# Kernel tuning notes

Measured on AMD Instinct MI355X. Metric: run time of the kernel, lower is better.

## Reference

```python
import jax, jax.numpy as jnp
import numpy as np
from jax import lax

B, T, EPROJS, DUNITS, ATT_DIM = 32, 2048, 1024, 1024, 512
ACONV_CHANS, ACONV_FILTS = 10, 100
KSIZE = 2 * ACONV_FILTS + 1  # 201
SCALING = 2.0


def setup_inputs() -> dict:
    key = jax.random.key(0)
    ks = jax.random.split(key, 16)
    lengths = jax.random.randint(ks[1], (B,), T // 2, T + 1, dtype=jnp.int32)
    # normalized uniform initial attention over valid frames (as in module's init branch)
    mask = jnp.arange(T)[None, :] < lengths[:, None]
    att_prev = mask.astype(jnp.float32) / lengths[:, None].astype(jnp.float32)
    s_e = 1.0 / np.sqrt(EPROJS)
    s_d = 1.0 / np.sqrt(DUNITS)
    s_a = 1.0 / np.sqrt(ATT_DIM)
    s_c = 1.0 / np.sqrt(ACONV_CHANS)
    return {
        "enc_hs_pad": jax.random.normal(ks[0], (B, T, EPROJS), jnp.float32),
        "enc_hs_len": lengths,
        "dec_z": jax.random.normal(ks[2], (B, DUNITS), jnp.float32),
        "att_prev": att_prev,
        "att_h": jax.random.normal(ks[3], (B, ATT_DIM), jnp.float32) * 0.1,
        "att_c": jax.random.normal(ks[4], (B, ATT_DIM), jnp.float32) * 0.1,
        "W_enc": jax.random.uniform(ks[5], (EPROJS, ATT_DIM), jnp.float32, -s_e, s_e),
        "b_enc": jax.random.uniform(ks[6], (ATT_DIM,), jnp.float32, -s_e, s_e),
        "W_dec": jax.random.uniform(ks[7], (DUNITS, ATT_DIM), jnp.float32, -s_d, s_d),
        "W_conv": jax.random.uniform(ks[8], (ACONV_CHANS, 1, KSIZE), jnp.float32, -0.1, 0.1),
        "W_ih": jax.random.uniform(ks[9], (4 * ATT_DIM, ACONV_CHANS), jnp.float32, -s_a, s_a),
        "W_hh": jax.random.uniform(ks[10], (4 * ATT_DIM, ATT_DIM), jnp.float32, -s_a, s_a),
        "W_g": jax.random.uniform(ks[11], (ATT_DIM, 1), jnp.float32, -s_a, s_a),
        "b_g": jax.random.uniform(ks[12], (1,), jnp.float32, -s_a, s_a),
    }


def reference(enc_hs_pad, enc_hs_len, dec_z, att_prev, att_h, att_c,
              W_enc, b_enc, W_dec, W_conv, W_ih, W_hh, W_g, b_g):
    # pre_compute_enc_h = mlp_enc(enc_h): (B, T, A)
    pre_enc = jnp.einsum("bte,ea->bta", enc_hs_pad, W_enc) + b_enc

    # location conv over previous attention: (B,1,T) -> (B,C,T)
    conv = lax.conv_general_dilated(
        att_prev[:, None, :], W_conv,
        window_strides=(1,), padding=[(ACONV_FILTS, ACONV_FILTS)],
        dimension_numbers=("NCH", "OIH", "NCH"))
    # relu + global max-pool over T -> (B, C)
    conv_feat = jnp.max(jax.nn.relu(conv), axis=2)

    # LSTMCell (no bias), PyTorch gate order i, f, g, o
    gates = conv_feat @ W_ih.T + att_h @ W_hh.T  # (B, 4A)
    i, f, g, o = jnp.split(gates, 4, axis=1)
    c_new = jax.nn.sigmoid(f) * att_c + jax.nn.sigmoid(i) * jnp.tanh(g)
    h_new = jax.nn.sigmoid(o) * jnp.tanh(c_new)

    dec_t = dec_z @ W_dec  # (B, A)
    # scoring: gvec(tanh(att_h + pre_enc + dec)) -> (B, T)
    e = (jnp.tanh(h_new[:, None, :] + pre_enc + dec_t[:, None, :]) @ W_g)[..., 0] + b_g[0]

    pad_mask = jnp.arange(e.shape[1])[None, :] >= enc_hs_len[:, None]
    e = jnp.where(pad_mask, -jnp.inf, e)
    w = jax.nn.softmax(SCALING * e, axis=1)  # (B, T)

    c = jnp.einsum("bt,bte->be", w, enc_hs_pad)  # (B, EPROJS)
    return c, w, h_new, c_new
```

## Files before the change

### kernel.cpp

```cpp
#include <hip/hip_runtime.h>
#include <hip/hip_bf16.h>
#include <cstddef>

#define BB      32
#define TT_ALL  2048
#define EPROJS  1024
#define DUNITS  1024
#define ATT     512
#define CH      10
#define KS      201
#define FILT    100

#define OFF_C   0
#define OFF_W   (BB*EPROJS)
#define OFF_H   (OFF_W + BB*TT_ALL)
#define OFF_CN  (OFF_H + BB*ATT)

#define WS_CF    0
#define WS_V     512
#define WS_E     16896
#define WS_WF    82432
#define WS_WT    147968
#define WS_PART  410112
#define WS_GP    672256
#define WS_DP    803328

typedef __attribute__((ext_vector_type(8))) short short8;
typedef __attribute__((ext_vector_type(4))) float f32x4;

__device__ __forceinline__ float sigm(float x) { return 1.f / (1.f + expf(-x)); }
__device__ __forceinline__ unsigned short f2bf(float f) {
  unsigned u = __float_as_uint(f);
  return (unsigned short)((u + 0x7FFFu + ((u >> 16) & 1u)) >> 16);
}
__device__ __forceinline__ ushort2 f2bf2(float a, float b) {
  __hip_bfloat162 h = __float22bfloat162_rn(float2{a, b});
  return *reinterpret_cast<ushort2*>(&h);
}

__global__ __launch_bounds__(64) void k_wprepF(const float* __restrict__ W,
                                               unsigned short* __restrict__ WTF) {
  const int r16 = blockIdx.x >> 5, ks = blockIdx.x & 31;
  const int l = threadIdx.x;
  const int a = r16 * 16 + (l & 15);
  const int e0 = ks * 32 + (l >> 4) * 8;
  union { short8 s; unsigned short h[8]; } r;
#pragma unroll
  for (int j = 0; j < 8; ++j) r.h[j] = f2bf(W[(size_t)(e0 + j) * ATT + a]);
  *reinterpret_cast<short8*>(&WTF[((size_t)(r16 * 32 + ks) * 64 + l) * 8]) = r.s;
}

__global__ __launch_bounds__(256) void k_conv(const float* __restrict__ att_prev,
                                              const float* __restrict__ W_conv,
                                              float* __restrict__ conv_feat) {
  const int b  = blockIdx.x / CH;
  const int ch = blockIdx.x % CH;
  __shared__ float sprev[TT_ALL + 2 * FILT];
  __shared__ float sw[KS];
  __shared__ float red[4];
  const int tid = threadIdx.x;
  for (int i = tid; i < TT_ALL + 2 * FILT; i += 256) {
    int t = i - FILT;
    sprev[i] = (t >= 0 && t < TT_ALL) ? att_prev[b * TT_ALL + t] : 0.f;
  }
  for (int i = tid; i < KS; i += 256) sw[i] = W_conv[ch * KS + i];
  __syncthreads();
  float m = 0.f;
  for (int t = tid; t < TT_ALL; t += 256) {
    float s = 0.f;
    for (int k = 0; k < KS; ++k) s = fmaf(sprev[t + k], sw[k], s);
    m = fmaxf(m, s);
  }
  for (int off = 32; off; off >>= 1) m = fmaxf(m, __shfl_xor(m, off, 64));
  if ((tid & 63) == 0) red[tid >> 6] = m;
  __syncthreads();
  if (tid == 0)
    conv_feat[b * CH + ch] = fmaxf(fmaxf(red[0], red[1]), fmaxf(red[2], red[3]));
}

__global__ __launch_bounds__(256) void k_gates(const float* __restrict__ att_h,
                                               const float* __restrict__ W_hh,
                                               float* __restrict__ gp) {
  const int jt = blockIdx.x >> 1;
  const int sp = blockIdx.x & 1;
  const int j0 = jt * 64;
  const int k0 = sp * 256;
  const int tid = threadIdx.x;
  const int al = tid & 63, bg = tid >> 6;
  __shared__ float sW[64][65];
  __shared__ float sH[32][64];
  float acc[8];
#pragma unroll
  for (int i = 0; i < 8; ++i) acc[i] = 0.f;
  for (int kc = 0; kc < 256; kc += 64) {
    __syncthreads();
#pragma unroll
    for (int i = 0; i < 4; ++i) {
      const int f = tid + i * 256;
      const int r = f >> 4, q = f & 15;
      const float4 w4 = *reinterpret_cast<const float4*>(
          &W_hh[(size_t)(j0 + r) * ATT + k0 + kc + q * 4]);
      sW[r][q * 4 + 0] = w4.x; sW[r][q * 4 + 1] = w4.y;
      sW[r][q * 4 + 2] = w4.z; sW[r][q * 4 + 3] = w4.w;
    }
#pragma unroll
    for (int i = 0; i < 2; ++i) {
      const int g = tid + i * 256;
      const int r = g >> 4, q = g & 15;
      *reinterpret_cast<float4*>(&sH[r][q * 4]) = *reinterpret_cast<const float4*>(
          &att_h[(size_t)r * ATT + k0 + kc + q * 4]);
    }
    __syncthreads();
#pragma unroll 16
    for (int k = 0; k < 64; ++k) {
      const float w = sW[al][k];
#pragma unroll
      for (int bb = 0; bb < 8; ++bb)
        acc[bb] = fmaf(w, sH[bg * 8 + bb][k], acc[bb]);
    }
  }
#pragma unroll
  for (int bb = 0; bb < 8; ++bb)
    gp[((size_t)(sp * 32 + bg * 8 + bb)) * (4 * ATT) + j0 + al] = acc[bb];
}

__global__ __launch_bounds__(256) void k_dec(const float* __restrict__ dec_z,
                                             const float* __restrict__ W_dec,
                                             float* __restrict__ dp) {
  const int at = blockIdx.x >> 1;
  const int sp = blockIdx.x & 1;
  const int a0 = at * 64;
  const int d0 = sp * 512;
  const int tid = threadIdx.x;
  const int al = tid & 63, bg = tid >> 6;
  __shared__ float sW[64][64];
  __shared__ float sZ[32][64];
  float acc[8];
#pragma unroll
  for (int i = 0; i < 8; ++i) acc[i] = 0.f;
  for (int dc = 0; dc < 512; dc += 64) {
    __syncthreads();
#pragma unroll
    for (int i = 0; i < 4; ++i) {
      const int f = tid + i * 256;
      const int r = f >> 4, q = f & 15;
      *reinterpret_cast<float4*>(&sW[r][q * 4]) = *reinterpret_cast<const float4*>(
          &W_dec[(size_t)(d0 + dc + r) * ATT + a0 + q * 4]);
    }
#pragma unroll
    for (int i = 0; i < 2; ++i) {
      const int g = tid + i * 256;
      const int r = g >> 4, q = g & 15;
      *reinterpret_cast<float4*>(&sZ[r][q * 4]) = *reinterpret_cast<const float4*>(
          &dec_z[(size_t)r * DUNITS + d0 + dc + q * 4]);
    }
    __syncthreads();
#pragma unroll 16
    for (int d = 0; d < 64; ++d) {
      const float w = sW[d][al];
#pragma unroll
      for (int bb = 0; bb < 8; ++bb)
        acc[bb] = fmaf(sZ[bg * 8 + bb][d], w, acc[bb]);
    }
  }
#pragma unroll
  for (int bb = 0; bb < 8; ++bb)
    dp[((size_t)(sp * 32 + bg * 8 + bb)) * ATT + a0 + al] = acc[bb];
}

__global__ __launch_bounds__(256) void k_lstm_v(const float* __restrict__ gp,
                                                const float* __restrict__ dp,
                                                const float* __restrict__ conv_feat,
                                                const float* __restrict__ W_ih,
                                                const float* __restrict__ att_c,
                                                float* __restrict__ v,
                                                float* __restrict__ out) {
  const int b = blockIdx.x, tid = threadIdx.x;
  __shared__ float scf[CH];
  if (tid < CH) scf[tid] = conv_feat[b * CH + tid];
  __syncthreads();
  for (int a = tid; a < ATT; a += 256) {
    float g4[4];
#pragma unroll
    for (int q = 0; q < 4; ++q) {
      const int j = q * ATT + a;
      float g = gp[(size_t)b * (4 * ATT) + j] + gp[(size_t)(32 + b) * (4 * ATT) + j];
#pragma unroll
      for (int c = 0; c < CH; ++c) g = fmaf(scf[c], W_ih[(size_t)j * CH + c], g);
      g4[q] = g;
    }
    const float ig = sigm(g4[0]);
    const float fg = sigm(g4[1]);
    const float gg = tanhf(g4[2]);
    const float og = sigm(g4[3]);
    const float cN = fg * att_c[b * ATT + a] + ig * gg;
    const float hN = og * tanhf(cN);
    out[OFF_H + b * ATT + a]  = hN;
    out[OFF_CN + b * ATT + a] = cN;
    v[b * ATT + a] = hN + dp[(size_t)b * ATT + a] + dp[(size_t)(32 + b) * ATT + a];
  }
}

__global__ __launch_bounds__(512, 2) void k_score_mfma(const float* __restrict__ enc,
                                                       const unsigned short* __restrict__ WTF,
                                                       const float* __restrict__ b_enc,
                                                       const float* __restrict__ W_g,
                                                       const float* __restrict__ v,
                                                       const int* __restrict__ lens,
                                                       float* __restrict__ e_out) {
  const int b  = blockIdx.x >> 5;
  const int tt = blockIdx.x & 31;
  const int t0 = tt * 64;
  if (t0 >= lens[b]) return;
  const int tid = threadIdx.x;
  const int lane = tid & 63, wn = tid >> 6;
  const int l15 = lane & 15, l4 = lane >> 4;

  __shared__ unsigned short sA[2][64][40];
  __shared__ float red[64][8];

  const int rowS = tid >> 3, qS = tid & 7;
  const float* pAg = enc + ((size_t)b * TT_ALL + t0 + rowS) * EPROJS + qS * 4;
  const unsigned short* pBf = WTF + (size_t)(wn * 4) * 32 * 512 + (size_t)lane * 8;

  f32x4 acc[4][4];
#pragma unroll
  for (int m = 0; m < 4; ++m)
#pragma unroll
    for (int n = 0; n < 4; ++n) acc[m][n] = (f32x4){0.f, 0.f, 0.f, 0.f};

  float4 a0 = *reinterpret_cast<const float4*>(pAg);

  for (int ks = 0; ks < 32; ++ks) {
    const int buf = ks & 1;
    {
      const ushort2 h0 = f2bf2(a0.x, a0.y), h1 = f2bf2(a0.z, a0.w);
      ushort4 h; h.x = h0.x; h.y = h0.y; h.z = h1.x; h.w = h1.y;
      *reinterpret_cast<ushort4*>(&sA[buf][rowS][qS * 4]) = h;
    }
    __syncthreads();
    if (ks + 1 < 32)
      a0 = *reinterpret_cast<const float4*>(pAg + (ks + 1) * 32);
    short8 bfr[4];
#pragma unroll
    for (int n = 0; n < 4; ++n)
      bfr[n] = *reinterpret_cast<const short8*>(pBf + (size_t)(n * 32 + ks) * 512);
    short8 af[4];
#pragma unroll
    for (int m = 0; m < 4; ++m)
      af[m] = *reinterpret_cast<const short8*>(&sA[buf][16 * m + l15][l4 * 8]);
#pragma unroll
    for (int n = 0; n < 4; ++n)
#pragma unroll
      for (int m = 0; m < 4; ++m)
        acc[m][n] = __builtin_amdgcn_mfma_f32_16x16x32_bf16(af[m], bfr[n], acc[m][n], 0, 0, 0);
  }

  float rp[4][4];
#pragma unroll
  for (int m = 0; m < 4; ++m)
#pragma unroll
    for (int j = 0; j < 4; ++j) rp[m][j] = 0.f;
#pragma unroll
  for (int n = 0; n < 4; ++n) {
    const int a = wn * 64 + 16 * n + l15;
    const float va = v[b * ATT + a] + b_enc[a];
    const float wg = W_g[a];
#pragma unroll
    for (int m = 0; m < 4; ++m)
#pragma unroll
      for (int j = 0; j < 4; ++j) {
        const float x = acc[m][n][j] + va;
        const float th = 1.f - 2.f / (__expf(2.f * x) + 1.f);
        rp[m][j] = fmaf(th, wg, rp[m][j]);
      }
  }
#pragma unroll
  for (int m = 0; m < 4; ++m)
#pragma unroll
    for (int j = 0; j < 4; ++j) {
      float s = rp[m][j];
      s += __shfl_xor(s, 1, 64);
      s += __shfl_xor(s, 2, 64);
      s += __shfl_xor(s, 4, 64);
      s += __shfl_xor(s, 8, 64);
      rp[m][j] = s;
    }
  __syncthreads();
  if (l15 == 0) {
#pragma unroll
    for (int m = 0; m < 4; ++m)
#pragma unroll
      for (int j = 0; j < 4; ++j)
        red[16 * m + l4 * 4 + j][wn] = rp[m][j];
  }
  __syncthreads();
  if (tid < 64) {
    float s = 0.f;
#pragma unroll
    for (int q = 0; q < 8; ++q) s += red[tid][q];
    e_out[b * TT_ALL + t0 + tid] = s;
  }
}

__global__ __launch_bounds__(256) void k_softmax(const float* __restrict__ e,
                                                 const int* __restrict__ lens,
                                                 float* __restrict__ wf,
                                                 float* __restrict__ out) {
  const int b = blockIdx.x, tid = threadIdx.x, len = lens[b];
  __shared__ float sbuf[4];
  float vals[8];
  float m = -1e30f;
#pragma unroll
  for (int i = 0; i < 8; ++i) {
    const int t = tid + i * 256;
    const float x = (t < len) ? e[b * TT_ALL + t] : -1e30f;
    vals[i] = x;
    m = fmaxf(m, x);
  }
  for (int off = 32; off; off >>= 1) m = fmaxf(m, __shfl_xor(m, off, 64));
  if ((tid & 63) == 0) sbuf[tid >> 6] = m;
  __syncthreads();
  m = fmaxf(fmaxf(sbuf[0], sbuf[1]), fmaxf(sbuf[2], sbuf[3]));
  __syncthreads();
  float s = 0.f;
#pragma unroll
  for (int i = 0; i < 8; ++i) {
    const int t = tid + i * 256;
    const float p = (t < len) ? expf(2.f * (vals[i] - m)) : 0.f;
    vals[i] = p;
    s += p;
  }
  for (int off = 32; off; off >>= 1) s += __shfl_xor(s, off, 64);
  if ((tid & 63) == 0) sbuf[tid >> 6] = s;
  __syncthreads();
  s = sbuf[0] + sbuf[1] + sbuf[2] + sbuf[3];
  const float inv = 1.f / s;
#pragma unroll
  for (int i = 0; i < 8; ++i) {
    const int t = tid + i * 256;
    const float wv = vals[i] * inv;
    wf[b * TT_ALL + t] = wv;
    out[OFF_W + b * TT_ALL + t] = wv;
  }
}

__global__ __launch_bounds__(256) void k_ctx(const float* __restrict__ enc,
                                             const float* __restrict__ wf,
                                             const int* __restrict__ lens,
                                             float* __restrict__ part) {
  const int blk = blockIdx.x;
  const int b  = blk >> 5;
  const int et = (blk >> 3) & 3;
  const int tc = blk & 7;
  const int tid = threadIdx.x;
  const int e = et * 256 + tid;
  const int len = lens[b];
  const int tbeg = tc * 256;
  const int tend = min(tbeg + 256, len);
  float a0 = 0.f, a1 = 0.f;
  int t = tbeg;
  for (; t + 2 <= tend; t += 2) {
    a0 = fmaf(wf[b * TT_ALL + t + 0], enc[((size_t)b * TT_ALL + t + 0) * EPROJS + e], a0);
    a1 = fmaf(wf[b * TT_ALL + t + 1], enc[((size_t)b * TT_ALL + t + 1) * EPROJS + e], a1);
  }
  for (; t < tend; ++t)
    a0 = fmaf(wf[b * TT_ALL + t], enc[((size_t)b * TT_ALL + t) * EPROJS + e], a0);
  part[((size_t)b * 8 + tc) * EPROJS + e] = a0 + a1;
}

__global__ __launch_bounds__(256) void k_comb(const float* __restrict__ part,
                                              float* __restrict__ out) {
  const int b = blockIdx.x >> 2, et = blockIdx.x & 3;
  const int e = et * 256 + threadIdx.x;
  float s = 0.f;
#pragma unroll
  for (int tc = 0; tc < 8; ++tc) s += part[((size_t)b * 8 + tc) * EPROJS + e];
  out[OFF_C + b * EPROJS + e] = s;
}

extern "C" void kernel_launch(void* const* d_in, const int* in_sizes, int n_in,
                              void* d_out, int out_size, void* d_ws, size_t ws_size,
                              hipStream_t stream) {
  const float* enc      = (const float*)d_in[0];
  const int*   lens     = (const int*)d_in[1];
  const float* dec_z    = (const float*)d_in[2];
  const float* att_prev = (const float*)d_in[3];
  const float* att_h    = (const float*)d_in[4];
  const float* att_c    = (const float*)d_in[5];
  const float* W_enc    = (const float*)d_in[6];
  const float* b_enc    = (const float*)d_in[7];
  const float* W_dec    = (const float*)d_in[8];
  const float* W_conv   = (const float*)d_in[9];
  const float* W_ih     = (const float*)d_in[10];
  const float* W_hh     = (const float*)d_in[11];
  const float* W_g      = (const float*)d_in[12];
  const float* b_g      = (const float*)d_in[13];
  (void)b_g;
  float* out = (float*)d_out;
  float* ws  = (float*)d_ws;

  float* cf   = ws + WS_CF;
  float* v    = ws + WS_V;
  float* e_s  = ws + WS_E;
  float* wf   = ws + WS_WF;
  unsigned short* wtf = (unsigned short*)(ws + WS_WT);
  float* part = ws + WS_PART;
  float* gp   = ws + WS_GP;
  float* dp   = ws + WS_DP;

  k_wprepF    <<<32 * 32, 64, 0, stream>>>(W_enc, wtf);
  k_conv      <<<BB * CH, 256, 0, stream>>>(att_prev, W_conv, cf);
  k_gates     <<<64, 256, 0, stream>>>(att_h, W_hh, gp);
  k_dec       <<<16, 256, 0, stream>>>(dec_z, W_dec, dp);
  k_lstm_v    <<<BB, 256, 0, stream>>>(gp, dp, cf, W_ih, att_c, v, out);
  k_score_mfma<<<BB * 32, 512, 0, stream>>>(enc, wtf, b_enc, W_g, v, lens, e_s);
  k_softmax   <<<BB, 256, 0, stream>>>(e_s, lens, wf, out);
  k_ctx       <<<BB * 32, 256, 0, stream>>>(enc, wf, lens, part);
  k_comb      <<<BB * 4, 256, 0, stream>>>(part, out);
}
```

Before: 226.1 us.

## Stage half the K dimension of encoder tile in LDS per barrier

```diff
diff --git a/kernel.cpp b/kernel.cpp
--- a/kernel.cpp
+++ b/kernel.cpp
@@ -36,6 +36,12 @@
 __device__ __forceinline__ ushort2 f2bf2(float a, float b) {
   __hip_bfloat162 h = __float22bfloat162_rn(float2{a, b});
   return *reinterpret_cast<ushort2*>(&h);
+}
+__device__ __forceinline__ short8 pack_bf16x8(const float4 a, const float4 b) {
+  union { short8 s; ushort2 u[4]; } r;
+  r.u[0] = f2bf2(a.x, a.y); r.u[1] = f2bf2(a.z, a.w);
+  r.u[2] = f2bf2(b.x, b.y); r.u[3] = f2bf2(b.z, b.w);
+  return r.s;
 }
 
 __global__ __launch_bounds__(64) void k_wprepF(const float* __restrict__ W,
@@ -216,11 +222,11 @@
   const int lane = tid & 63, wn = tid >> 6;
   const int l15 = lane & 15, l4 = lane >> 4;
 
-  __shared__ unsigned short sA[2][64][40];
+  __shared__ unsigned short sA[64][520];
   __shared__ float red[64][8];
 
   const int rowS = tid >> 3, qS = tid & 7;
-  const float* pAg = enc + ((size_t)b * TT_ALL + t0 + rowS) * EPROJS + qS * 4;
+  const float* pAg = enc + ((size_t)b * TT_ALL + t0 + rowS) * EPROJS + qS * 64;
   const unsigned short* pBf = WTF + (size_t)(wn * 4) * 32 * 512 + (size_t)lane * 8;
 
   f32x4 acc[4][4];
@@ -229,31 +235,34 @@
 #pragma unroll
     for (int n = 0; n < 4; ++n) acc[m][n] = (f32x4){0.f, 0.f, 0.f, 0.f};
 
-  float4 a0 = *reinterpret_cast<const float4*>(pAg);
-
-  for (int ks = 0; ks < 32; ++ks) {
-    const int buf = ks & 1;
-    {
-      const ushort2 h0 = f2bf2(a0.x, a0.y), h1 = f2bf2(a0.z, a0.w);
-      ushort4 h; h.x = h0.x; h.y = h0.y; h.z = h1.x; h.w = h1.y;
-      *reinterpret_cast<ushort4*>(&sA[buf][rowS][qS * 4]) = h;
-    }
+  for (int h = 0; h < 2; ++h) {
+    float4 L[16];
+#pragma unroll
+    for (int j = 0; j < 16; ++j)
+      L[j] = *reinterpret_cast<const float4*>(pAg + h * 512 + j * 4);
+    if (h) __syncthreads();
+#pragma unroll
+    for (int j = 0; j < 8; ++j)
+      *reinterpret_cast<short8*>(&sA[rowS][qS * 64 + j * 8]) =
+          pack_bf16x8(L[2 * j], L[2 * j + 1]);
     __syncthreads();
-    if (ks + 1 < 32)
-      a0 = *reinterpret_cast<const float4*>(pAg + (ks + 1) * 32);
-    short8 bfr[4];
-#pragma unroll
-    for (int n = 0; n < 4; ++n)
-      bfr[n] = *reinterpret_cast<const short8*>(pBf + (size_t)(n * 32 + ks) * 512);
-    short8 af[4];
-#pragma unroll
-    for (int m = 0; m < 4; ++m)
-      af[m] = *reinterpret_cast<const short8*>(&sA[buf][16 * m + l15][l4 * 8]);
-#pragma unroll
-    for (int n = 0; n < 4; ++n)
+#pragma unroll 2
+    for (int ksl = 0; ksl < 16; ++ksl) {
+      const int ks = h * 16 + ksl;
+      short8 bfr[4];
+#pragma unroll
+      for (int n = 0; n < 4; ++n)
+        bfr[n] = *reinterpret_cast<const short8*>(pBf + (size_t)(n * 32 + ks) * 512);
+      short8 af[4];
 #pragma unroll
       for (int m = 0; m < 4; ++m)
-        acc[m][n] = __builtin_amdgcn_mfma_f32_16x16x32_bf16(af[m], bfr[n], acc[m][n], 0, 0, 0);
+        af[m] = *reinterpret_cast<const short8*>(&sA[16 * m + l15][ksl * 32 + l4 * 8]);
+#pragma unroll
+      for (int n = 0; n < 4; ++n)
+#pragma unroll
+        for (int m = 0; m < 4; ++m)
+          acc[m][n] = __builtin_amdgcn_mfma_f32_16x16x32_bf16(af[m], bfr[n], acc[m][n], 0, 0, 0);
+    }
   }
 
   float rp[4][4];
```

Measured after the change: 234.5 us. 3.7% more time.
